# Kernel optimization log

Measured on AMD Instinct MI355X. Metric: run time of the kernel, lower is better.

The kernel has to match this reference:

```python
import jax, jax.numpy as jnp
import numpy as np

# --- constants mirroring init_kwargs ---
DIM = 1024
N_HEADS = 16
N_KV_HEADS = 4
HEAD_DIM = DIM // N_HEADS          # 64
REP = N_HEADS // N_KV_HEADS        # 4
ROPE_THETA = 10000.0
WINDOW = 512
N_GLOBAL = 64
EPS = 1e-6


def setup_inputs() -> dict:
    key = jax.random.key(0)
    ks = jax.random.split(key, 7)
    B, L = 2, 2048
    x = jax.random.normal(ks[0], (B, L, DIM), dtype=jnp.float32)
    s = 0.02
    wq = jax.random.normal(ks[1], (DIM, N_HEADS * HEAD_DIM), dtype=jnp.float32) * s
    wk = jax.random.normal(ks[2], (DIM, N_KV_HEADS * HEAD_DIM), dtype=jnp.float32) * s
    wv = jax.random.normal(ks[3], (DIM, N_KV_HEADS * HEAD_DIM), dtype=jnp.float32) * s
    wo = jax.random.normal(ks[4], (N_HEADS * HEAD_DIM, DIM), dtype=jnp.float32) * s
    gq = jnp.ones((HEAD_DIM,), dtype=jnp.float32) + 0.01 * jax.random.normal(ks[5], (HEAD_DIM,), dtype=jnp.float32)
    gk = jnp.ones((HEAD_DIM,), dtype=jnp.float32) + 0.01 * jax.random.normal(ks[6], (HEAD_DIM,), dtype=jnp.float32)
    return {"x": x, "wq": wq, "wk": wk, "wv": wv, "wo": wo, "gq": gq, "gk": gk}


def _rmsnorm(t, g):
    # QKNorm: RMS norm over head_dim with learnable per-dim scale
    return t * jax.lax.rsqrt(jnp.mean(t * t, axis=-1, keepdims=True) + EPS) * g


def _rope(t, cos, sin):
    # t: [B,H,L,hd]; complex RoPE over consecutive pairs (2i, 2i+1)
    t1 = t[..., 0::2]
    t2 = t[..., 1::2]
    o1 = t1 * cos - t2 * sin
    o2 = t1 * sin + t2 * cos
    return jnp.stack([o1, o2], axis=-1).reshape(t.shape)


def reference(x, wq, wk, wv, wo, gq, gk):
    B, L, D = x.shape
    q = (x @ wq).reshape(B, L, N_HEADS, HEAD_DIM)
    k = (x @ wk).reshape(B, L, N_KV_HEADS, HEAD_DIM)
    v = (x @ wv).reshape(B, L, N_KV_HEADS, HEAD_DIM)
    q = _rmsnorm(q, gq)
    k = _rmsnorm(k, gk)
    q = q.transpose(0, 2, 1, 3)  # [B,H,L,hd]
    k = k.transpose(0, 2, 1, 3)
    v = v.transpose(0, 2, 1, 3)

    # RoPE frequencies (start_pos = 0)
    inv_freq = 1.0 / (ROPE_THETA ** (jnp.arange(0, HEAD_DIM, 2, dtype=jnp.float32) / HEAD_DIM))
    ang = jnp.arange(L, dtype=jnp.float32)[:, None] * inv_freq[None, :]  # [L, hd/2]
    cos, sin = jnp.cos(ang), jnp.sin(ang)
    q = _rope(q, cos, sin)
    k = _rope(k, cos, sin)

    # GQA: repeat kv heads (repeat_interleave on head dim)
    k = jnp.repeat(k, REP, axis=1)
    v = jnp.repeat(v, REP, axis=1)

    scores = jnp.einsum("bhqd,bhkd->bhqk", q, k) / np.sqrt(HEAD_DIM).astype(np.float32)

    # sliding-window + global-token causal mask
    half = WINDOW // 2
    i = jnp.arange(L)[:, None]
    j = jnp.arange(L)[None, :]
    m = (j <= i) & ((j >= i - half) | (j < N_GLOBAL))  # [L,L] bool
    scores = jnp.where(m[None, None], scores, -jnp.inf)

    attn = jax.nn.softmax(scores.astype(jnp.float32), axis=-1).astype(scores.dtype)
    out = jnp.einsum("bhqk,bhkd->bhqd", attn, v)
    out = out.transpose(0, 2, 1, 3).reshape(B, L, N_HEADS * HEAD_DIM)
    return out @ wo
```

## Files before the change

### kernel.cpp

```cpp
#include <hip/hip_runtime.h>
#include <hip/hip_bf16.h>

typedef __bf16 bf16x8 __attribute__((ext_vector_type(8)));
typedef __bf16 bf16x4 __attribute__((ext_vector_type(4)));
typedef float  f32x4  __attribute__((ext_vector_type(4)));
typedef short  s16x4  __attribute__((ext_vector_type(4)));

__device__ __forceinline__ __bf16 to_bf16(float f) {
    __hip_bfloat16 h = __float2bfloat16(f);
    return *reinterpret_cast<__bf16*>(&h);
}

__device__ __forceinline__ f32x4 mfma32(bf16x8 a, bf16x8 b, f32x4 c) {
    return __builtin_amdgcn_mfma_f32_16x16x32_bf16(a, b, c, 0, 0, 0);
}
__device__ __forceinline__ f32x4 mfma16(bf16x4 a, bf16x4 b, f32x4 c) {
#if __has_builtin(__builtin_amdgcn_mfma_f32_16x16x16_bf16)
    return __builtin_amdgcn_mfma_f32_16x16x16_bf16(a, b, c, 0, 0, 0);
#else
    return __builtin_amdgcn_mfma_f32_16x16x16bf16_1k(
        __builtin_bit_cast(s16x4, a), __builtin_bit_cast(s16x4, b), c, 0, 0, 0);
#endif
}

__device__ __forceinline__ void gload_lds16(const __bf16* g, __bf16* l) {
    __builtin_amdgcn_global_load_lds(
        (const __attribute__((address_space(1))) void*)g,
        (__attribute__((address_space(3))) void*)l, 16, 0, 0);
}


__global__ __launch_bounds__(256) void prep_k(const float* __restrict__ wq,
                                              const float* __restrict__ wk,
                                              const float* __restrict__ wv,
                                              const float* __restrict__ wo,
                                              const float* __restrict__ x,
                                              __bf16* __restrict__ WqkvT,
                                              __bf16* __restrict__ WoT,
                                              __bf16* __restrict__ xb) {
    int b = blockIdx.x, tid = threadIdx.x;
    if (b >= 2560) {
        int i = ((b - 2560) * 256 + tid) * 8;
        f32x4 a = *(const f32x4*)(x + i);
        f32x4 c = *(const f32x4*)(x + i + 4);
        bf16x8 h;
        h[0] = to_bf16(a.x); h[1] = to_bf16(a.y); h[2] = to_bf16(a.z); h[3] = to_bf16(a.w);
        h[4] = to_bf16(c.x); h[5] = to_bf16(c.y); h[6] = to_bf16(c.z); h[7] = to_bf16(c.w);
        *(bf16x8*)(xb + i) = h;
        return;
    }
    __shared__ float tile[32][33];
    const float* src; __bf16* dst; int N, idx;
    if (b < 1024)      { src = wq; dst = WqkvT;                        N = 1024; idx = b; }
    else if (b < 1280) { src = wk; dst = WqkvT + (size_t)1024 * 1024;  N = 256;  idx = b - 1024; }
    else if (b < 1536) { src = wv; dst = WqkvT + (size_t)1280 * 1024;  N = 256;  idx = b - 1280; }
    else               { src = wo; dst = WoT;                          N = 1024; idx = b - 1536; }
    int k0 = (idx & 31) * 32, n0 = (idx >> 5) * 32;
    int tx = tid & 31, ty = tid >> 5;
#pragma unroll
    for (int r = 0; r < 4; ++r) {
        int kk = ty + r * 8;
        tile[kk][tx] = src[(size_t)(k0 + kk) * N + n0 + tx];
    }
    __syncthreads();
#pragma unroll
    for (int r = 0; r < 4; ++r) {
        int nn = ty + r * 8;
        dst[(size_t)(n0 + nn) * 1024 + k0 + tx] = to_bf16(tile[tx][nn]);
    }
}

__global__ __launch_bounds__(256) void gemm_bf16_k(const __bf16* __restrict__ A,
                                                   const __bf16* __restrict__ BT,
                                                   float* __restrict__ C,
                                                   int K, int N) {
    __shared__ __bf16 lA[128 * 32];
    __shared__ __bf16 lB[64 * 32];
    int tid = threadIdx.x;
    int m0 = blockIdx.x * 128, n0 = blockIdx.y * 64;
    int wid = tid >> 6, lane = tid & 63;
    int wm = (wid & 1) * 64, wn = (wid >> 1) * 32;
    int lm = lane & 15, qd = lane >> 4;

    f32x4 acc[4][2] = {};

    for (int k0 = 0; k0 < K; k0 += 32) {
#pragma unroll
        for (int it = 0; it < 2; ++it) {
            int c = it * 256 + tid;
            int row = c >> 2, c8 = c & 3;
            __bf16* la = lA + (it * 256 + wid * 64) * 8;
            gload_lds16(A + (size_t)(m0 + row) * K + k0 + c8 * 8, la);
        }
        {
            int row = tid >> 2, c8 = tid & 3;
            __bf16* lb = lB + (wid * 64) * 8;
            gload_lds16(BT + (size_t)(n0 + row) * K + k0 + c8 * 8, lb);
        }
        __syncthreads();

        bf16x8 af[4], bfr[2];
#pragma unroll
        for (int t = 0; t < 4; ++t)
            af[t] = *(const bf16x8*)&lA[(wm + t * 16 + lm) * 32 + qd * 8];
#pragma unroll
        for (int j = 0; j < 2; ++j)
            bfr[j] = *(const bf16x8*)&lB[(wn + j * 16 + lm) * 32 + qd * 8];
#pragma unroll
        for (int ti = 0; ti < 4; ++ti)
#pragma unroll
            for (int tj = 0; tj < 2; ++tj)
                acc[ti][tj] = mfma32(af[ti], bfr[tj], acc[ti][tj]);
        __syncthreads();
    }

#pragma unroll
    for (int ti = 0; ti < 4; ++ti)
#pragma unroll
        for (int tj = 0; tj < 2; ++tj)
#pragma unroll
            for (int r = 0; r < 4; ++r) {
                int row = m0 + wm + ti * 16 + qd * 4 + r;
                int col = n0 + wn + tj * 16 + lm;
                C[(size_t)row * N + col] = acc[ti][tj][r];
            }
}

__global__ __launch_bounds__(256) void normv_k(const float* __restrict__ qkv,
                                               __bf16* __restrict__ Qb,
                                               __bf16* __restrict__ Kbl,
                                               __bf16* __restrict__ Vt,
                                               const float* __restrict__ gq,
                                               const float* __restrict__ gk) {
    __shared__ float tl[64][65];
    int b = blockIdx.x, tid = threadIdx.x;
    if (b < 20480) {
        int w = b * 4 + (tid >> 6);
        int lane = tid & 63;
        int t = w / 20, hs = w % 20;
        int pos = t & 2047, bb = t >> 11;
        bool isq = hs < 16;
        int col0 = isq ? hs * 64 : 1024 + (hs - 16) * 64;
        float g = isq ? gq[lane] : gk[lane];
        const float* p = qkv + (size_t)t * 1536 + col0;
        float v = p[lane];
        float ss = v * v;
#pragma unroll
        for (int o = 32; o; o >>= 1) ss += __shfl_xor(ss, o);
        float scale = rsqrtf(ss * (1.0f / 64.0f) + 1e-6f);
        v = v * scale * g;
        int i2 = lane >> 1;
        float ex = (float)(2 * i2) * (1.0f / 64.0f);
        float inv = expf(-ex * 9.210340371976184f);
        float ang = (float)pos * inv;
        float c = cosf(ang), s = sinf(ang);
        float pv = __shfl_xor(v, 1);
        float out = (lane & 1) ? (pv * s + v * c) : (v * c - pv * s);
        if (isq) {
            int kvh = hs >> 2, h4 = hs & 3;
            size_t off = (((((size_t)bb * 4 + kvh) * 128 + (pos >> 4)) * 4 + h4) * 16
                          + (pos & 15)) * 64 + lane;
            Qb[off] = to_bf16(out * 0.125f);
        } else {
            Kbl[(((size_t)bb * 4 + (hs - 16)) * 2048 + pos) * 64 + lane] = to_bf16(out);
        }
        return;
    }
    int b2 = b - 20480;
    int g = b2 >> 5, t0 = (b2 & 31) * 64;
    int bb = g >> 2, kvh = g & 3;
    int tx = tid & 63, ty = tid >> 6;
    const float* src = qkv + ((size_t)bb * 2048 + t0) * 1536 + 1280 + kvh * 64;
#pragma unroll
    for (int r = 0; r < 16; ++r) {
        int row = ty * 16 + r;
        tl[row][tx] = src[(size_t)row * 1536 + tx];
    }
    __syncthreads();
#pragma unroll
    for (int r = 0; r < 16; ++r) {
        int d = ty * 16 + r;
        Vt[((size_t)g * 64 + d) * 2048 + t0 + tx] = to_bf16(tl[tx][d]);
    }
}

__global__ __launch_bounds__(256) void attn_k(const __bf16* __restrict__ Qb,
                                              const __bf16* __restrict__ Kbl,
                                              const __bf16* __restrict__ Vt,
                                              __bf16* __restrict__ aout) {
    __shared__ __bf16 Kt[2][64 * 64];
    __shared__ __bf16 Vl[2][64 * 64];
    int tid = threadIdx.x, wid = tid >> 6, lane = tid & 63;
    int l15 = lane & 15, quad = lane >> 4;
    int qb = blockIdx.x, kvh = blockIdx.y, b = blockIdx.z;
    int iw = qb * 16;
    int g = b * 4 + kvh;
    int h = kvh * 4 + wid;
    int e7 = l15 & 7;

    const __bf16* qp = Qb + ((((size_t)g * 128 + qb) * 4 + wid) * 16 + l15) * 64 + quad * 8;
    bf16x8 qf0 = *(const bf16x8*)qp;
    bf16x8 qf1 = *(const bf16x8*)(qp + 32);

    int ts = (iw - 256) >> 6; if (ts < 1) ts = 1;
    int tmax = (iw + 15) >> 6;
    int n_all = (tmax >= ts) ? (tmax - ts + 2) : 1;

    const __bf16* Kg = Kbl + (size_t)g * 2048 * 64;
    const __bf16* Vg = Vt + (size_t)g * 64 * 2048;

    int r0 = tid >> 3, c0 = tid & 7;
    int kl0 = r0 * 64 + ((c0 ^ (r0 & 7)) * 8);
    int kl1 = kl0 + 32 * 64;

    bf16x8 kr0, kr1, vr0, vr1;
    auto stage_load = [&](int tt) {
        const __bf16* kb = Kg + (size_t)tt * 64 * 64;
        kr0 = *(const bf16x8*)(kb + r0 * 64 + c0 * 8);
        kr1 = *(const bf16x8*)(kb + (r0 + 32) * 64 + c0 * 8);
        const __bf16* vb = Vg + tt * 64 + c0 * 8;
        vr0 = *(const bf16x8*)(vb + (size_t)r0 * 2048);
        vr1 = *(const bf16x8*)(vb + (size_t)(r0 + 32) * 2048);
    };
    auto stage_write = [&](int buf) {
        *(bf16x8*)&Kt[buf][kl0] = kr0;
        *(bf16x8*)&Kt[buf][kl1] = kr1;
        *(bf16x8*)&Vl[buf][kl0] = vr0;
        *(bf16x8*)&Vl[buf][kl1] = vr1;
    };

    stage_load(0);
    stage_write(0);

    f32x4 o[4] = {};
    float mr = -1e30f, lrp = 0.f;
    int iq = iw + l15;

    for (int idx = 0; idx < n_all; ++idx) {
        int tt = (idx == 0) ? 0 : ts + idx - 1;
        if (idx + 1 < n_all) stage_load(ts + idx);
        __syncthreads();
        int buf = idx & 1;

        f32x4 s[4] = {};
#pragma unroll
        for (int nt = 0; nt < 4; ++nt) {
            const __bf16* kp = &Kt[buf][(nt * 16 + l15) * 64];
            bf16x8 k0 = *(const bf16x8*)(kp + ((quad ^ e7) * 8));
            bf16x8 k1 = *(const bf16x8*)(kp + (((quad + 4) ^ e7) * 8));
            s[nt] = mfma32(k0, qf0, s[nt]);
            s[nt] = mfma32(k1, qf1, s[nt]);
        }

        bool need_mask = (tt == tmax) || (tt >= 1 && tt * 64 < iw + 15 - 256);
        if (need_mask) {
#pragma unroll
            for (int nt = 0; nt < 4; ++nt)
#pragma unroll
                for (int r = 0; r < 4; ++r) {
                    int j = tt * 64 + nt * 16 + quad * 4 + r;
                    bool valid = (j <= iq) && ((j >= iq - 256) || (j < 64));
                    s[nt][r] = valid ? s[nt][r] : -1e30f;
                }
        }

        float mx = -1e30f;
#pragma unroll
        for (int nt = 0; nt < 4; ++nt)
#pragma unroll
            for (int r = 0; r < 4; ++r) mx = fmaxf(mx, s[nt][r]);
        mx = fmaxf(mx, __shfl_xor(mx, 16));
        mx = fmaxf(mx, __shfl_xor(mx, 32));
        float mn = fmaxf(mr, mx);
        float alpha = __expf(mr - mn);
        mr = mn;

        float ps = 0.f;
        bf16x4 pb[4];
#pragma unroll
        for (int nt = 0; nt < 4; ++nt)
#pragma unroll
            for (int r = 0; r < 4; ++r) {
                float pv = __expf(s[nt][r] - mn);
                ps += pv;
                pb[nt][r] = to_bf16(pv);
            }
        lrp = lrp * alpha + ps;

#pragma unroll
        for (int dt = 0; dt < 4; ++dt) {
            o[dt] *= alpha;
            const __bf16* vp = &Vl[buf][(dt * 16 + l15) * 64];
#pragma unroll
            for (int nt = 0; nt < 4; ++nt) {
                int c8 = 2 * nt + (quad >> 1);
                bf16x4 va = *(const bf16x4*)(vp + ((c8 ^ e7) * 8) + (quad & 1) * 4);
                o[dt] = mfma16(va, pb[nt], o[dt]);
            }
        }

        if (idx + 1 < n_all) stage_write((idx + 1) & 1);
    }

    lrp += __shfl_xor(lrp, 16);
    lrp += __shfl_xor(lrp, 32);
    float inv = 1.f / lrp;
    __syncthreads();
    __bf16* pr = &Kt[0][wid * 16 * 64];
#pragma unroll
    for (int dt = 0; dt < 4; ++dt)
#pragma unroll
        for (int r = 0; r < 4; ++r) {
            int e = dt * 16 + quad * 4 + r;
            int c8 = e >> 3;
            pr[l15 * 64 + ((c8 ^ e7) * 8) + (e & 7)] = to_bf16(o[dt][r] * inv);
        }
    bf16x8 o0 = *(const bf16x8*)(pr + l15 * 64 + (((2 * quad) ^ e7) * 8));
    bf16x8 o1 = *(const bf16x8*)(pr + l15 * 64 + (((2 * quad + 1) ^ e7) * 8));
    __bf16* op = aout + ((size_t)b * 2048 + iw + l15) * 1024 + h * 64 + quad * 16;
    *(bf16x8*)op = o0;
    *(bf16x8*)(op + 8) = o1;
}

extern "C" void kernel_launch(void* const* d_in, const int* in_sizes, int n_in,
                              void* d_out, int out_size, void* d_ws, size_t ws_size,
                              hipStream_t stream) {
    const float* x  = (const float*)d_in[0];
    const float* wq = (const float*)d_in[1];
    const float* wk = (const float*)d_in[2];
    const float* wv = (const float*)d_in[3];
    const float* wo = (const float*)d_in[4];
    const float* gq = (const float*)d_in[5];
    const float* gk = (const float*)d_in[6];
    float* out = (float*)d_out;

    char* ws = (char*)d_ws;
    float*  qkv   = (float*)ws;
    __bf16* WqkvT = (__bf16*)(ws + 25165824);
    __bf16* WoT   = (__bf16*)(ws + 28311552);
    __bf16* xb_ao = (__bf16*)(ws + 30408704);
    __bf16* Kbl   = (__bf16*)(ws + 38797312);
    __bf16* Vt    = (__bf16*)(ws + 40894464);
    __bf16* Qb    = (__bf16*)(ws + 42991616);

    dim3 tb(256);
    prep_k<<<4608, tb, 0, stream>>>(wq, wk, wv, wo, x, WqkvT, WoT, xb_ao);
    gemm_bf16_k<<<dim3(32, 24), tb, 0, stream>>>(xb_ao, WqkvT, qkv, 1024, 1536);
    normv_k<<<20736, tb, 0, stream>>>(qkv, Qb, Kbl, Vt, gq, gk);
    attn_k<<<dim3(128, 4, 2), tb, 0, stream>>>(Qb, Kbl, Vt, xb_ao);
    gemm_bf16_k<<<dim3(32, 16), tb, 0, stream>>>(xb_ao, WoT, out, 1024, 1024);
}
```

Baseline: 169.5 us.

## Fuse QK RMSNorm, RoPE and V transpose into the QKV GEMM epilogue

Result: faster. 159.6 us (-5.8%).

```diff
diff --git a/kernel.cpp b/kernel.cpp
--- a/kernel.cpp
+++ b/kernel.cpp
@@ -70,6 +70,128 @@
     }
 }
 
+__global__ __launch_bounds__(256) void gemmqkv_k(const __bf16* __restrict__ A,
+                                                 const __bf16* __restrict__ BT,
+                                                 const float* __restrict__ gq,
+                                                 const float* __restrict__ gk,
+                                                 __bf16* __restrict__ Qb,
+                                                 __bf16* __restrict__ Kbl,
+                                                 __bf16* __restrict__ Vt) {
+    __shared__ __bf16 lA[128 * 32];
+    __shared__ __bf16 lB[64 * 32];
+    __shared__ float ssp[2][128];
+    __shared__ __bf16 tv[64 * 136];
+    const int K = 1024;
+    int tid = threadIdx.x;
+    int m0 = blockIdx.x * 128, n0 = blockIdx.y * 64;
+    int head = n0 >> 6;
+    int wid = tid >> 6, lane = tid & 63;
+    int wm = (wid & 1) * 64, wn = (wid >> 1) * 32;
+    int lm = lane & 15, qd = lane >> 4;
+
+    f32x4 acc[4][2] = {};
+
+    for (int k0 = 0; k0 < K; k0 += 32) {
+#pragma unroll
+        for (int it = 0; it < 2; ++it) {
+            int c = it * 256 + tid;
+            int row = c >> 2, c8 = c & 3;
+            __bf16* la = lA + (it * 256 + wid * 64) * 8;
+            gload_lds16(A + (size_t)(m0 + row) * K + k0 + c8 * 8, la);
+        }
+        {
+            int row = tid >> 2, c8 = tid & 3;
+            __bf16* lb = lB + (wid * 64) * 8;
+            gload_lds16(BT + (size_t)(n0 + row) * K + k0 + c8 * 8, lb);
+        }
+        __syncthreads();
+
+        bf16x8 af[4], bfr[2];
+#pragma unroll
+        for (int t = 0; t < 4; ++t)
+            af[t] = *(const bf16x8*)&lA[(wm + t * 16 + lm) * 32 + qd * 8];
+#pragma unroll
+        for (int j = 0; j < 2; ++j)
+            bfr[j] = *(const bf16x8*)&lB[(wn + j * 16 + lm) * 32 + qd * 8];
+#pragma unroll
+        for (int ti = 0; ti < 4; ++ti)
+#pragma unroll
+            for (int tj = 0; tj < 2; ++tj)
+                acc[ti][tj] = mfma32(af[ti], bfr[tj], acc[ti][tj]);
+        __syncthreads();
+    }
+
+    if (head < 20) {
+#pragma unroll
+        for (int ti = 0; ti < 4; ++ti)
+#pragma unroll
+            for (int r = 0; r < 4; ++r) {
+                float sq = acc[ti][0][r] * acc[ti][0][r] + acc[ti][1][r] * acc[ti][1][r];
+                sq += __shfl_xor(sq, 1);
+                sq += __shfl_xor(sq, 2);
+                sq += __shfl_xor(sq, 4);
+                sq += __shfl_xor(sq, 8);
+                if (lm == 0) ssp[wid >> 1][wm + ti * 16 + qd * 4 + r] = sq;
+            }
+        __syncthreads();
+
+        bool isq = head < 16;
+#pragma unroll
+        for (int ti = 0; ti < 4; ++ti)
+#pragma unroll
+            for (int r = 0; r < 4; ++r) {
+                int row = wm + ti * 16 + qd * 4 + r;
+                int t = m0 + row;
+                int pos = t & 2047, bb = t >> 11;
+                float ss = ssp[0][row] + ssp[1][row];
+                float scale = rsqrtf(ss * (1.0f / 64.0f) + 1e-6f);
+#pragma unroll
+                for (int tj = 0; tj < 2; ++tj) {
+                    int col = wn + tj * 16 + lm;
+                    float g = isq ? gq[col] : gk[col];
+                    float v = acc[ti][tj][r] * scale * g;
+                    float ex = (float)(2 * (col >> 1)) * (1.0f / 64.0f);
+                    float invf = expf(-ex * 9.210340371976184f);
+                    float ang = (float)pos * invf;
+                    float c = cosf(ang), s = sinf(ang);
+                    float pv = __shfl_xor(v, 1);
+                    float outv = (col & 1) ? (pv * s + v * c) : (v * c - pv * s);
+                    if (isq) {
+                        int kvh = head >> 2, h4 = head & 3;
+                        size_t off = (((((size_t)bb * 4 + kvh) * 128 + (pos >> 4)) * 4 + h4) * 16
+                                      + (pos & 15)) * 64 + col;
+                        Qb[off] = to_bf16(outv * 0.125f);
+                    } else {
+                        int kvg = head - 16;
+                        Kbl[(((size_t)bb * 4 + kvg) * 2048 + pos) * 64 + col] = to_bf16(outv);
+                    }
+                }
+            }
+    } else {
+#pragma unroll
+        for (int ti = 0; ti < 4; ++ti)
+#pragma unroll
+            for (int tj = 0; tj < 2; ++tj)
+#pragma unroll
+                for (int r = 0; r < 4; ++r) {
+                    int row = wm + ti * 16 + qd * 4 + r;
+                    int col = wn + tj * 16 + lm;
+                    tv[col * 136 + row] = to_bf16(acc[ti][tj][r]);
+                }
+        __syncthreads();
+        int bb = m0 >> 11, kvg = head - 20;
+        size_t gg = (size_t)bb * 4 + kvg;
+        int pos0 = m0 & 2047;
+#pragma unroll
+        for (int p = 0; p < 4; ++p) {
+            int d = p * 16 + (tid >> 4);
+            int tok = (tid & 15) * 8;
+            bf16x8 vvv = *(const bf16x8*)&tv[d * 136 + tok];
+            *(bf16x8*)(Vt + (gg * 64 + d) * 2048 + pos0 + tok) = vvv;
+        }
+    }
+}
+
 __global__ __launch_bounds__(256) void gemm_bf16_k(const __bf16* __restrict__ A,
                                                    const __bf16* __restrict__ BT,
                                                    float* __restrict__ C,
@@ -124,64 +246,6 @@
                 int col = n0 + wn + tj * 16 + lm;
                 C[(size_t)row * N + col] = acc[ti][tj][r];
             }
-}
-
-__global__ __launch_bounds__(256) void normv_k(const float* __restrict__ qkv,
-                                               __bf16* __restrict__ Qb,
-                                               __bf16* __restrict__ Kbl,
-                                               __bf16* __restrict__ Vt,
-                                               const float* __restrict__ gq,
-                                               const float* __restrict__ gk) {
-    __shared__ float tl[64][65];
-    int b = blockIdx.x, tid = threadIdx.x;
-    if (b < 20480) {
-        int w = b * 4 + (tid >> 6);
-        int lane = tid & 63;
-        int t = w / 20, hs = w % 20;
-        int pos = t & 2047, bb = t >> 11;
-        bool isq = hs < 16;
-        int col0 = isq ? hs * 64 : 1024 + (hs - 16) * 64;
-        float g = isq ? gq[lane] : gk[lane];
-        const float* p = qkv + (size_t)t * 1536 + col0;
-        float v = p[lane];
-        float ss = v * v;
-#pragma unroll
-        for (int o = 32; o; o >>= 1) ss += __shfl_xor(ss, o);
-        float scale = rsqrtf(ss * (1.0f / 64.0f) + 1e-6f);
-        v = v * scale * g;
-        int i2 = lane >> 1;
-        float ex = (float)(2 * i2) * (1.0f / 64.0f);
-        float inv = expf(-ex * 9.210340371976184f);
-        float ang = (float)pos * inv;
-        float c = cosf(ang), s = sinf(ang);
-        float pv = __shfl_xor(v, 1);
-        float out = (lane & 1) ? (pv * s + v * c) : (v * c - pv * s);
-        if (isq) {
-            int kvh = hs >> 2, h4 = hs & 3;
-            size_t off = (((((size_t)bb * 4 + kvh) * 128 + (pos >> 4)) * 4 + h4) * 16
-                          + (pos & 15)) * 64 + lane;
-            Qb[off] = to_bf16(out * 0.125f);
-        } else {
-            Kbl[(((size_t)bb * 4 + (hs - 16)) * 2048 + pos) * 64 + lane] = to_bf16(out);
-        }
-        return;
-    }
-    int b2 = b - 20480;
-    int g = b2 >> 5, t0 = (b2 & 31) * 64;
-    int bb = g >> 2, kvh = g & 3;
-    int tx = tid & 63, ty = tid >> 6;
-    const float* src = qkv + ((size_t)bb * 2048 + t0) * 1536 + 1280 + kvh * 64;
-#pragma unroll
-    for (int r = 0; r < 16; ++r) {
-        int row = ty * 16 + r;
-        tl[row][tx] = src[(size_t)row * 1536 + tx];
-    }
-    __syncthreads();
-#pragma unroll
-    for (int r = 0; r < 16; ++r) {
-        int d = ty * 16 + r;
-        Vt[((size_t)g * 64 + d) * 2048 + t0 + tx] = to_bf16(tl[tx][d]);
-    }
 }
 
 __global__ __launch_bounds__(256) void attn_k(const __bf16* __restrict__ Qb,
@@ -335,18 +399,16 @@
     float* out = (float*)d_out;
 
     char* ws = (char*)d_ws;
-    float*  qkv   = (float*)ws;
-    __bf16* WqkvT = (__bf16*)(ws + 25165824);
-    __bf16* WoT   = (__bf16*)(ws + 28311552);
-    __bf16* xb_ao = (__bf16*)(ws + 30408704);
-    __bf16* Kbl   = (__bf16*)(ws + 38797312);
-    __bf16* Vt    = (__bf16*)(ws + 40894464);
-    __bf16* Qb    = (__bf16*)(ws + 42991616);
+    __bf16* WqkvT = (__bf16*)ws;
+    __bf16* WoT   = (__bf16*)(ws + 3145728);
+    __bf16* xb_ao = (__bf16*)(ws + 5242880);
+    __bf16* Kbl   = (__bf16*)(ws + 13631488);
+    __bf16* Vt    = (__bf16*)(ws + 15728640);
+    __bf16* Qb    = (__bf16*)(ws + 17825792);
 
     dim3 tb(256);
     prep_k<<<4608, tb, 0, stream>>>(wq, wk, wv, wo, x, WqkvT, WoT, xb_ao);
-    gemm_bf16_k<<<dim3(32, 24), tb, 0, stream>>>(xb_ao, WqkvT, qkv, 1024, 1536);
-    normv_k<<<20736, tb, 0, stream>>>(qkv, Qb, Kbl, Vt, gq, gk);
+    gemmqkv_k<<<dim3(32, 24), tb, 0, stream>>>(xb_ao, WqkvT, gq, gk, Qb, Kbl, Vt);
     attn_k<<<dim3(128, 4, 2), tb, 0, stream>>>(Qb, Kbl, Vt, xb_ao);
     gemm_bf16_k<<<dim3(32, 16), tb, 0, stream>>>(xb_ao, WoT, out, 1024, 1024);
 }
```
